# Kernel optimization log

Hardware: AMD Instinct MI355X
Metric: run time of the kernel (lower is better)

The kernel has to match this reference:

```python
import jax, jax.numpy as jnp
import numpy as np

NUM_GROUPS = 32
EPS = 1e-5


def setup_inputs() -> dict:
    key = jax.random.key(0)
    ks = jax.random.split(key, 6)
    B, C, H, W = 8, 128, 64, 64
    d = C // 8
    x = jax.random.normal(ks[0], (B, C, H, W), dtype=jnp.float32)
    # conv 1x1 weights stored as [out_ch, in_ch]; scaled like torch kaiming-uniform-ish
    s = 1.0 / np.sqrt(C)
    return {
        "x": x,
        "gn_w": jnp.ones((C,), jnp.float32),
        "gn_b": jnp.zeros((C,), jnp.float32),
        "q_w": jax.random.normal(ks[1], (d, C), jnp.float32) * s,
        "q_b": jnp.zeros((d,), jnp.float32),
        "k_w": jax.random.normal(ks[2], (d, C), jnp.float32) * s,
        "k_b": jnp.zeros((d,), jnp.float32),
        "v_w": jax.random.normal(ks[3], (C, C), jnp.float32) * s,
        "v_b": jnp.zeros((C,), jnp.float32),
        "p_w": jax.random.normal(ks[4], (C, C), jnp.float32) * s,
        "p_b": jnp.zeros((C,), jnp.float32),
    }


def _group_norm(x, w, b):
    B, C, H, W = x.shape
    g = NUM_GROUPS
    xr = x.reshape(B, g, C // g, H, W)
    mu = xr.mean(axis=(2, 3, 4), keepdims=True)
    var = xr.var(axis=(2, 3, 4), keepdims=True)
    xn = ((xr - mu) * jax.lax.rsqrt(var + EPS)).reshape(B, C, H, W)
    return xn * w[None, :, None, None] + b[None, :, None, None]


def reference(x, gn_w, gn_b, q_w, q_b, k_w, k_b, v_w, v_b, p_w, p_b):
    B, C, H, W = x.shape
    N = H * W
    h_ = _group_norm(x, gn_w, gn_b)            # [B,C,H,W]
    hf = h_.reshape(B, C, N)                   # flatten spatial
    # 1x1 convs == channel matmuls
    q = jnp.einsum('dc,bcn->bnd', q_w, hf) + q_b[None, None, :]   # [B,N,d]
    k = jnp.einsum('dc,bcn->bnd', k_w, hf) + k_b[None, None, :]   # [B,N,d]
    v = jnp.einsum('ec,bcn->ben', v_w, hf) + v_b[None, :, None]   # [B,C,N]
    d = q.shape[-1]
    scale = jnp.asarray(int(d) ** (-0.5), x.dtype)
    attn = jnp.einsum('bid,bjd->bij', q, k) * scale               # [B,N,N]
    attn = jax.nn.softmax(attn, axis=-1)
    a = jnp.einsum('bcj,bij->bci', v, attn)                       # [B,C,N]
    proj = jnp.einsum('ec,bcn->ben', p_w, a) + p_b[None, :, None]
    return x + proj.reshape(B, C, H, W)
```

## Files before the change

kernel.cpp:

```cpp
#include <hip/hip_runtime.h>
#include <math.h>


typedef short v8s __attribute__((ext_vector_type(8)));
typedef float v16f __attribute__((ext_vector_type(16)));

__device__ __forceinline__ unsigned short f2bf_rne(float f) {
  unsigned u = __float_as_uint(f);
  u += 0x7fffu + ((u >> 16) & 1u);
  return (unsigned short)(u >> 16);
}

__device__ __forceinline__ v8s mk8(unsigned a, unsigned b, unsigned c, unsigned d) {
  union { unsigned u[4]; v8s s; } x;
  x.u[0] = a; x.u[1] = b; x.u[2] = c; x.u[3] = d;
  return x.s;
}

__device__ __forceinline__ unsigned pack_trunc(float hi, float lo) {
  return __builtin_amdgcn_perm(__float_as_uint(hi), __float_as_uint(lo), 0x07060302u);
}

__device__ __forceinline__ void cp16_async(const unsigned short* g, unsigned short* l) {
  __builtin_amdgcn_global_load_lds(
      (const __attribute__((address_space(1))) unsigned int*)g,
      (__attribute__((address_space(3))) unsigned int*)l, 16, 0, 0);
}

#define VT(b, n, c) (((((size_t)(b) * 256 + ((n) >> 4)) << 7) + (c)) * 16 + ((n) & 15))

#define WSB_MURS   0u
#define WSB_WCATB  4096u
#define WSB_BCAT   49152u
#define WSB_PWB    65536u
#define WSB_QBF    131072u
#define WSB_KBF    1310720u
#define WSB_VBF    2621440u
#define WSB_ABF    11534336u

__global__ __launch_bounds__(512)
void gnprep_kernel(const float* __restrict__ x, float* __restrict__ mu_rs,
                   const float* __restrict__ qw, const float* __restrict__ qb,
                   const float* __restrict__ kw, const float* __restrict__ kb,
                   const float* __restrict__ vw, const float* __restrict__ vb,
                   const float* __restrict__ pw,
                   unsigned short* __restrict__ wcatb, float* __restrict__ bcat,
                   unsigned short* __restrict__ pwb) {
  const int id = blockIdx.x;
  {
    const float qs = 0.36067376022224085f;
    int idx = id * 512 + threadIdx.x;
    if (idx < 160 * 128) {
      int o = idx >> 7, c = idx & 127;
      float val;
      if (o < 16)       val = qw[o * 128 + c] * qs;
      else if (o < 32)  val = kw[(o - 16) * 128 + c];
      else              val = vw[(o - 32) * 128 + c];
      wcatb[idx] = f2bf_rne(val);
    } else if (idx < 160 * 128 + 160) {
      int o = idx - 160 * 128;
      bcat[o] = (o < 16) ? qb[o] * qs : (o < 32) ? kb[o - 16] : vb[o - 32];
    } else if (idx < 160 * 128 + 160 + 128 * 128) {
      int j = idx - (160 * 128 + 160);
      pwb[j] = f2bf_rne(pw[j]);
    }
  }
  const int bg = (id & 7) * 32 + (id >> 3);
  const float4* xp = (const float4*)(x + (size_t)bg * 16384);
  float s = 0.f, ss = 0.f;
#pragma unroll
  for (int u = 0; u < 8; ++u) {
    int i = threadIdx.x + u * 512;
    float4 v = xp[i];
    s  += v.x + v.y + v.z + v.w;
    ss += v.x * v.x + v.y * v.y + v.z * v.z + v.w * v.w;
  }
  for (int off = 32; off > 0; off >>= 1) {
    s  += __shfl_down(s, off, 64);
    ss += __shfl_down(ss, off, 64);
  }
  __shared__ float red[16];
  int lane = threadIdx.x & 63, wid = threadIdx.x >> 6;
  if (lane == 0) { red[wid * 2] = s; red[wid * 2 + 1] = ss; }
  __syncthreads();
  if (threadIdx.x == 0) {
    float S = 0.f, SS = 0.f;
    for (int w = 0; w < 8; ++w) { S += red[w * 2]; SS += red[w * 2 + 1]; }
    float mu  = S * (1.0f / 16384.0f);
    float var = SS * (1.0f / 16384.0f) - mu * mu;
    float rs  = rsqrtf(var + 1e-5f);
    mu_rs[bg * 2]     = mu;
    mu_rs[bg * 2 + 1] = rs;
  }
}

__global__ __launch_bounds__(512)
void qkv_kernel(const float* __restrict__ x, const float* __restrict__ gnw,
                const float* __restrict__ gnb, const float* __restrict__ mu_rs,
                const unsigned short* __restrict__ wcatb, const float* __restrict__ bcat,
                unsigned short* __restrict__ qTb, unsigned short* __restrict__ kbf,
                unsigned short* __restrict__ vbf) {
  __shared__ float scs[128], shs[128], bsh[160];
  const int id = blockIdx.x;
  const int b = id & 7, nb = (id >> 3) << 6;
  const int t = threadIdx.x;
  const int w = t >> 6, lane = t & 63, h = lane >> 5, l = lane & 31;
  const int nsub = w & 1, og = w >> 1;
  if (t < 128) {
    float mu = mu_rs[(b * 32 + (t >> 2)) * 2];
    float rs = mu_rs[(b * 32 + (t >> 2)) * 2 + 1];
    float gw = gnw[t], gb = gnb[t];
    scs[t] = rs * gw; shs[t] = gb - mu * rs * gw;
  }
  if (t < 160) bsh[t] = bcat[t];
  __syncthreads();

  const int n = nb + nsub * 32 + l;
  const float* xb = x + ((size_t)b * 128 << 12);
  const int otbase = (og == 0) ? 0 : og + 1;

  float xv[64];
#pragma unroll
  for (int ks = 0; ks < 8; ++ks)
#pragma unroll
    for (int p = 0; p < 8; ++p)
      xv[ks * 8 + p] = xb[((size_t)(ks * 16 + 8 * h + p) << 12) + n];

  v16f acc[2];
#pragma unroll
  for (int a2 = 0; a2 < 2; ++a2)
#pragma unroll
    for (int r = 0; r < 16; ++r) acc[a2][r] = 0.f;

#pragma unroll
  for (int ks = 0; ks < 8; ++ks) {
    const int c0 = ks * 16 + 8 * h;
    unsigned fd[4];
#pragma unroll
    for (int p = 0; p < 4; ++p) {
      int ca = c0 + 2 * p;
      float h0 = xv[ks * 8 + 2 * p]     * scs[ca]     + shs[ca];
      float h1 = xv[ks * 8 + 2 * p + 1] * scs[ca + 1] + shs[ca + 1];
      fd[p] = (unsigned)f2bf_rne(h0) | ((unsigned)f2bf_rne(h1) << 16);
    }
    v8s bf = mk8(fd[0], fd[1], fd[2], fd[3]);
    {
      v8s af = *(const v8s*)(wcatb + (otbase * 32 + l) * 128 + ks * 16 + 8 * h);
      acc[0] = __builtin_amdgcn_mfma_f32_32x32x16_bf16(af, bf, acc[0], 0, 0, 0);
    }
    if (og == 0) {
      v8s af = *(const v8s*)(wcatb + (32 + l) * 128 + ks * 16 + 8 * h);
      acc[1] = __builtin_amdgcn_mfma_f32_32x32x16_bf16(af, bf, acc[1], 0, 0, 0);
    }
  }

  if (og == 0) {
    const size_t nqk = ((size_t)b * 4096 + n) << 4;
#pragma unroll
    for (int r = 0; r < 16; ++r) {
      int o = 4 * h + (r & 3) + 8 * (r >> 2);
      unsigned short bv = f2bf_rne(acc[0][r] + bsh[o]);
      if (o < 16) qTb[((size_t)(b * 16 + o) << 12) + n] = bv;
      else        kbf[nqk + o - 16] = bv;
    }
#pragma unroll
    for (int r = 0; r < 16; ++r) {
      int o = 32 + 4 * h + (r & 3) + 8 * (r >> 2);
      vbf[VT(b, n, o - 32)] = f2bf_rne(acc[1][r] + bsh[o]);
    }
  } else {
#pragma unroll
    for (int r = 0; r < 16; ++r) {
      int o = otbase * 32 + 4 * h + (r & 3) + 8 * (r >> 2);
      vbf[VT(b, n, o - 32)] = f2bf_rne(acc[0][r] + bsh[o]);
    }
  }
}

__global__ __launch_bounds__(256)
void attn_kernel(const unsigned short* __restrict__ qTb,
                 const unsigned short* __restrict__ kbf,
                 const unsigned short* __restrict__ vbf,
                 unsigned short* __restrict__ abf) {
  __shared__ alignas(16) unsigned short smem[2][8192];
  __shared__ float l_lds[64];

  const int id = blockIdx.x;
  const int b = id & 7, i0 = (id >> 3) << 6;
  const int t = threadIdx.x;
  const int w = t >> 6, lane = t & 63, h = lane >> 5, l = lane & 31;
  const int jsub = w & 1, ihalf = w >> 1;

  const unsigned short* kg = kbf + ((size_t)b << 16);
  const unsigned short* vg = vbf + ((size_t)b << 19);

  const int iglob = i0 + ihalf * 32 + l;
  unsigned qd[4];
#pragma unroll
  for (int e = 0; e < 4; ++e) {
    unsigned lo = qTb[((size_t)(b * 16 + 8 * h + 2 * e) << 12) + iglob];
    unsigned hi = qTb[((size_t)(b * 16 + 8 * h + 2 * e + 1) << 12) + iglob];
    qd[e] = lo | (hi << 16);
  }
  const v8s qf = mk8(qd[0], qd[1], qd[2], qd[3]);

  v16f zc;
#pragma unroll
  for (int r = 0; r < 16; ++r) zc[r] = 0.f;
  v16f acc[4];
#pragma unroll
  for (int ct = 0; ct < 4; ++ct)
#pragma unroll
    for (int r = 0; r < 16; ++r) acc[ct][r] = 0.f;
  float ls = 0.f;

  if (t < 64) l_lds[t] = 0.f;

#pragma unroll
  for (int u = 0; u < 4; ++u)
    cp16_async(vg + (size_t)(w * 2048 + u * 512) + lane * 8,
               &smem[0][w * 2048 + u * 512]);
  __syncthreads();

  for (int tile = 0; tile < 64; ++tile) {
    const int tn = (tile + 1) & 63;
    unsigned short* const cur = smem[tile & 1];
    unsigned short* const nxt = smem[(tile + 1) & 1];

#pragma unroll
    for (int u = 0; u < 4; ++u)
      cp16_async(vg + (size_t)tn * 8192 + (w * 2048 + u * 512) + lane * 8,
                 &nxt[w * 2048 + u * 512]);

    v8s kf = *(const v8s*)(kg + (((size_t)(tile * 64 + jsub * 32 + l)) << 4) + 8 * h);

    v16f st = __builtin_amdgcn_mfma_f32_32x32x16_bf16(kf, qf, zc, 0, 0, 0);
    float pe[16];
#pragma unroll
    for (int r = 0; r < 16; ++r) { pe[r] = __builtin_amdgcn_exp2f(st[r]); ls += pe[r]; }
    unsigned G[8];
#pragma unroll
    for (int g = 0; g < 4; ++g) {
      G[2 * g]     = pack_trunc(pe[4 * g + 1], pe[4 * g]);
      G[2 * g + 1] = pack_trunc(pe[4 * g + 3], pe[4 * g + 2]);
    }
    unsigned S0 = h ? G[0] : G[2], S1 = h ? G[1] : G[3];
    unsigned S2 = h ? G[4] : G[6], S3 = h ? G[5] : G[7];
    unsigned R0 = (unsigned)__shfl_xor((int)S0, 32, 64);
    unsigned R1 = (unsigned)__shfl_xor((int)S1, 32, 64);
    unsigned R2 = (unsigned)__shfl_xor((int)S2, 32, 64);
    unsigned R3 = (unsigned)__shfl_xor((int)S3, 32, 64);
    v8s pf0 = h ? mk8(R0, R1, G[2], G[3]) : mk8(G[0], G[1], R0, R1);
    v8s pf1 = h ? mk8(R2, R3, G[6], G[7]) : mk8(G[4], G[5], R2, R3);

#pragma unroll
    for (int ct = 0; ct < 4; ++ct) {
      v8s vf0 = *(const v8s*)(&cur[((jsub * 2) * 128 + ct * 32 + l) * 16 + 8 * h]);
      v8s vf1 = *(const v8s*)(&cur[((jsub * 2 + 1) * 128 + ct * 32 + l) * 16 + 8 * h]);
      acc[ct] = __builtin_amdgcn_mfma_f32_32x32x16_bf16(vf0, pf0, acc[ct], 0, 0, 0);
      acc[ct] = __builtin_amdgcn_mfma_f32_32x32x16_bf16(vf1, pf1, acc[ct], 0, 0, 0);
    }

    __syncthreads();
  }

  atomicAdd(&l_lds[ihalf * 32 + l], ls);
  __syncthreads();
  float* const ov = (float*)smem;
  const float li = 1.f / l_lds[ihalf * 32 + l];
#pragma unroll
  for (int pass = 0; pass < 2; ++pass) {
    const int cta = pass * 2, ctb = pass * 2 + 1;
    if (jsub == 1) {
#pragma unroll
      for (int k = 0; k < 2; ++k) {
        const int ct = pass * 2 + k;
#pragma unroll
        for (int q = 0; q < 4; ++q) {
          float4 v4 = {acc[ct][4 * q], acc[ct][4 * q + 1],
                       acc[ct][4 * q + 2], acc[ct][4 * q + 3]};
          *(float4*)&ov[((k * 2 + ihalf) * 32 + l) * 36 + 4 * h + 8 * q] = v4;
        }
      }
    }
    __syncthreads();
    if (jsub == 0) {
#pragma unroll
      for (int k = 0; k < 2; ++k) {
        const int ct = pass * 2 + k;
#pragma unroll
        for (int q = 0; q < 4; ++q) {
          float4 v4 = *(float4*)&ov[((k * 2 + ihalf) * 32 + l) * 36 + 4 * h + 8 * q];
          acc[ct][4 * q]     += v4.x;
          acc[ct][4 * q + 1] += v4.y;
          acc[ct][4 * q + 2] += v4.z;
          acc[ct][4 * q + 3] += v4.w;
        }
#pragma unroll
        for (int r = 0; r < 16; ++r) {
          int c = ct * 32 + 4 * h + (r & 3) + 8 * (r >> 2);
          abf[((size_t)(b * 128 + c) << 12) + (size_t)(i0 + ihalf * 32 + l)] =
              f2bf_rne(acc[ct][r] * li);
        }
      }
    }
    __syncthreads();
  }
}

__global__ __launch_bounds__(512)
void proj_kernel(const unsigned short* __restrict__ abf, const unsigned short* __restrict__ pwb,
                 const float* __restrict__ pb, const float* __restrict__ x,
                 float* __restrict__ out) {
  __shared__ float pbs[128];
  const int id = blockIdx.x;
  const int b = id & 7, nb = (id >> 3) << 6;
  const int t = threadIdx.x;
  const int w = t >> 6, lane = t & 63, h = lane >> 5, l = lane & 31;
  const int nsub = w & 1, ot = w >> 1;
  if (t < 128) pbs[t] = pb[t];
  __syncthreads();

  const int n = nb + nsub * 32 + l;
  const unsigned short* ab = abf + (((size_t)b * 128) << 12);

  unsigned short av[64];
#pragma unroll
  for (int ks = 0; ks < 8; ++ks)
#pragma unroll
    for (int p = 0; p < 8; ++p)
      av[ks * 8 + p] = ab[((size_t)(ks * 16 + 8 * h + p) << 12) + n];

  v16f acc;
#pragma unroll
  for (int r = 0; r < 16; ++r) acc[r] = 0.f;

#pragma unroll
  for (int ks = 0; ks < 8; ++ks) {
    unsigned fd[4];
#pragma unroll
    for (int p = 0; p < 4; ++p)
      fd[p] = (unsigned)av[ks * 8 + 2 * p] | ((unsigned)av[ks * 8 + 2 * p + 1] << 16);
    v8s bf = mk8(fd[0], fd[1], fd[2], fd[3]);
    v8s af = *(const v8s*)(pwb + (ot * 32 + l) * 128 + ks * 16 + 8 * h);
    acc = __builtin_amdgcn_mfma_f32_32x32x16_bf16(af, bf, acc, 0, 0, 0);
  }

#pragma unroll
  for (int r = 0; r < 16; ++r) {
    int e = ot * 32 + 4 * h + (r & 3) + 8 * (r >> 2);
    size_t idx = ((size_t)(b * 128 + e) << 12) + n;
    out[idx] = acc[r] + pbs[e] + x[idx];
  }
}

extern "C" void kernel_launch(void* const* d_in, const int* in_sizes, int n_in,
                              void* d_out, int out_size, void* d_ws, size_t ws_size,
                              hipStream_t stream) {
  const float* x   = (const float*)d_in[0];
  const float* gnw = (const float*)d_in[1];
  const float* gnb = (const float*)d_in[2];
  const float* qw  = (const float*)d_in[3];
  const float* qb  = (const float*)d_in[4];
  const float* kw  = (const float*)d_in[5];
  const float* kb  = (const float*)d_in[6];
  const float* vw  = (const float*)d_in[7];
  const float* vb  = (const float*)d_in[8];
  const float* pw  = (const float*)d_in[9];
  const float* pb  = (const float*)d_in[10];
  float* out = (float*)d_out;
  char* ws = (char*)d_ws;

  float* mu_rs = (float*)(ws + WSB_MURS);
  unsigned short* wcatb = (unsigned short*)(ws + WSB_WCATB);
  float* bcat = (float*)(ws + WSB_BCAT);
  unsigned short* pwb = (unsigned short*)(ws + WSB_PWB);
  unsigned short* qTb = (unsigned short*)(ws + WSB_QBF);
  unsigned short* kbf = (unsigned short*)(ws + WSB_KBF);
  unsigned short* vbf = (unsigned short*)(ws + WSB_VBF);
  unsigned short* abf = (unsigned short*)(ws + WSB_ABF);

  hipLaunchKernelGGL(gnprep_kernel, dim3(256), dim3(512), 0, stream,
                     x, mu_rs, qw, qb, kw, kb, vw, vb, pw, wcatb, bcat, pwb);
  hipLaunchKernelGGL(qkv_kernel, dim3(512), dim3(512), 0, stream,
                     x, gnw, gnb, mu_rs, wcatb, bcat, qTb, kbf, vbf);
  hipLaunchKernelGGL(attn_kernel, dim3(512), dim3(256), 0, stream,
                     qTb, kbf, vbf, abf);
  hipLaunchKernelGGL(proj_kernel, dim3(512), dim3(512), 0, stream,
                     abf, pwb, pb, x, out);
}
```

Before: 172.6 us.

## Restructure attention to share V tiles across query halves and reblock A layout

The attention kernel now has each wave process both 32-row query halves against its own 32-key slice, with 128-key tiles staged through padded LDS using register loads instead of async global-to-LDS copies. The goal is to reuse each V fragment across two MFMAs, halve the tile count and avoid bank conflicts. The final reduction across the four waves now uses LDS float atomics. The intermediate attention output is stored in a channel-blocked layout (8 channels contiguous per position), so the projection kernel can load v8s fragments directly instead of making scattered 2-byte loads. In exchange, the kernel keeps twice as many accumulators live (register pressure), loses the double-buffered prefetch overlap, and pays for the atomic reduction.

```diff
diff --git a/kernel.cpp b/kernel.cpp
--- a/kernel.cpp
+++ b/kernel.cpp
@@ -21,13 +21,8 @@
   return __builtin_amdgcn_perm(__float_as_uint(hi), __float_as_uint(lo), 0x07060302u);
 }
 
-__device__ __forceinline__ void cp16_async(const unsigned short* g, unsigned short* l) {
-  __builtin_amdgcn_global_load_lds(
-      (const __attribute__((address_space(1))) unsigned int*)g,
-      (__attribute__((address_space(3))) unsigned int*)l, 16, 0, 0);
-}
-
 #define VT(b, n, c) (((((size_t)(b) * 256 + ((n) >> 4)) << 7) + (c)) * 16 + ((n) & 15))
+#define AB(b, c, n) ((((size_t)((b) * 16 + ((c) >> 3)) << 12) + (n)) * 8 + ((c) & 7))
 
 #define WSB_MURS   0u
 #define WSB_WCATB  4096u
@@ -177,134 +172,151 @@
   }
 }
 
+#define VSD 20
+
 __global__ __launch_bounds__(256)
 void attn_kernel(const unsigned short* __restrict__ qTb,
                  const unsigned short* __restrict__ kbf,
                  const unsigned short* __restrict__ vbf,
                  unsigned short* __restrict__ abf) {
-  __shared__ alignas(16) unsigned short smem[2][8192];
+  __shared__ alignas(16) unsigned short vlds[1024 * VSD];
   __shared__ float l_lds[64];
+  float* const ov = (float*)vlds;
 
   const int id = blockIdx.x;
   const int b = id & 7, i0 = (id >> 3) << 6;
   const int t = threadIdx.x;
   const int w = t >> 6, lane = t & 63, h = lane >> 5, l = lane & 31;
-  const int jsub = w & 1, ihalf = w >> 1;
 
   const unsigned short* kg = kbf + ((size_t)b << 16);
   const unsigned short* vg = vbf + ((size_t)b << 19);
 
-  const int iglob = i0 + ihalf * 32 + l;
-  unsigned qd[4];
+  unsigned qd0[4], qd1[4];
 #pragma unroll
   for (int e = 0; e < 4; ++e) {
-    unsigned lo = qTb[((size_t)(b * 16 + 8 * h + 2 * e) << 12) + iglob];
-    unsigned hi = qTb[((size_t)(b * 16 + 8 * h + 2 * e + 1) << 12) + iglob];
-    qd[e] = lo | (hi << 16);
-  }
-  const v8s qf = mk8(qd[0], qd[1], qd[2], qd[3]);
+    size_t rowa = (size_t)(b * 16 + 8 * h + 2 * e) << 12;
+    size_t rowb = (size_t)(b * 16 + 8 * h + 2 * e + 1) << 12;
+    unsigned lo0 = qTb[rowa + i0 + l],      hi0 = qTb[rowb + i0 + l];
+    unsigned lo1 = qTb[rowa + i0 + 32 + l], hi1 = qTb[rowb + i0 + 32 + l];
+    qd0[e] = lo0 | (hi0 << 16);
+    qd1[e] = lo1 | (hi1 << 16);
+  }
+  const v8s qf0 = mk8(qd0[0], qd0[1], qd0[2], qd0[3]);
+  const v8s qf1 = mk8(qd1[0], qd1[1], qd1[2], qd1[3]);
 
   v16f zc;
 #pragma unroll
   for (int r = 0; r < 16; ++r) zc[r] = 0.f;
-  v16f acc[4];
+  v16f acc[4][2];
 #pragma unroll
   for (int ct = 0; ct < 4; ++ct)
 #pragma unroll
-    for (int r = 0; r < 16; ++r) acc[ct][r] = 0.f;
-  float ls = 0.f;
+    for (int ih = 0; ih < 2; ++ih)
+#pragma unroll
+      for (int r = 0; r < 16; ++r) acc[ct][ih][r] = 0.f;
+  float ls0 = 0.f, ls1 = 0.f;
+
+  const int sc = t >> 1, shalf = (t & 1) * 8;
 
   if (t < 64) l_lds[t] = 0.f;
 
-#pragma unroll
-  for (int u = 0; u < 4; ++u)
-    cp16_async(vg + (size_t)(w * 2048 + u * 512) + lane * 8,
-               &smem[0][w * 2048 + u * 512]);
-  __syncthreads();
-
-  for (int tile = 0; tile < 64; ++tile) {
-    const int tn = (tile + 1) & 63;
-    unsigned short* const cur = smem[tile & 1];
-    unsigned short* const nxt = smem[(tile + 1) & 1];
-
-#pragma unroll
-    for (int u = 0; u < 4; ++u)
-      cp16_async(vg + (size_t)tn * 8192 + (w * 2048 + u * 512) + lane * 8,
-                 &nxt[w * 2048 + u * 512]);
-
-    v8s kf = *(const v8s*)(kg + (((size_t)(tile * 64 + jsub * 32 + l)) << 4) + 8 * h);
-
-    v16f st = __builtin_amdgcn_mfma_f32_32x32x16_bf16(kf, qf, zc, 0, 0, 0);
-    float pe[16];
-#pragma unroll
-    for (int r = 0; r < 16; ++r) { pe[r] = __builtin_amdgcn_exp2f(st[r]); ls += pe[r]; }
-    unsigned G[8];
-#pragma unroll
-    for (int g = 0; g < 4; ++g) {
-      G[2 * g]     = pack_trunc(pe[4 * g + 1], pe[4 * g]);
-      G[2 * g + 1] = pack_trunc(pe[4 * g + 3], pe[4 * g + 2]);
-    }
-    unsigned S0 = h ? G[0] : G[2], S1 = h ? G[1] : G[3];
-    unsigned S2 = h ? G[4] : G[6], S3 = h ? G[5] : G[7];
-    unsigned R0 = (unsigned)__shfl_xor((int)S0, 32, 64);
-    unsigned R1 = (unsigned)__shfl_xor((int)S1, 32, 64);
-    unsigned R2 = (unsigned)__shfl_xor((int)S2, 32, 64);
-    unsigned R3 = (unsigned)__shfl_xor((int)S3, 32, 64);
-    v8s pf0 = h ? mk8(R0, R1, G[2], G[3]) : mk8(G[0], G[1], R0, R1);
-    v8s pf1 = h ? mk8(R2, R3, G[6], G[7]) : mk8(G[4], G[5], R2, R3);
-
-#pragma unroll
-    for (int ct = 0; ct < 4; ++ct) {
-      v8s vf0 = *(const v8s*)(&cur[((jsub * 2) * 128 + ct * 32 + l) * 16 + 8 * h]);
-      v8s vf1 = *(const v8s*)(&cur[((jsub * 2 + 1) * 128 + ct * 32 + l) * 16 + 8 * h]);
-      acc[ct] = __builtin_amdgcn_mfma_f32_32x32x16_bf16(vf0, pf0, acc[ct], 0, 0, 0);
-      acc[ct] = __builtin_amdgcn_mfma_f32_32x32x16_bf16(vf1, pf1, acc[ct], 0, 0, 0);
-    }
+  for (int tile = 0; tile < 32; ++tile) {
+    v8s s[8];
+#pragma unroll
+    for (int u = 0; u < 8; ++u)
+      s[u] = *(const v8s*)(vg + (size_t)tile * 16384 + u * 2048 + sc * 16 + shalf);
+    v8s kf = *(const v8s*)(kg + (((size_t)(tile * 128 + w * 32 + l)) << 4) + 8 * h);
 
     __syncthreads();
-  }
-
-  atomicAdd(&l_lds[ihalf * 32 + l], ls);
-  __syncthreads();
-  float* const ov = (float*)smem;
-  const float li = 1.f / l_lds[ihalf * 32 + l];
-#pragma unroll
-  for (int pass = 0; pass < 2; ++pass) {
-    const int cta = pass * 2, ctb = pass * 2 + 1;
-    if (jsub == 1) {
-#pragma unroll
-      for (int k = 0; k < 2; ++k) {
-        const int ct = pass * 2 + k;
-#pragma unroll
-        for (int q = 0; q < 4; ++q) {
-          float4 v4 = {acc[ct][4 * q], acc[ct][4 * q + 1],
-                       acc[ct][4 * q + 2], acc[ct][4 * q + 3]};
-          *(float4*)&ov[((k * 2 + ihalf) * 32 + l) * 36 + 4 * h + 8 * q] = v4;
-        }
+
+#pragma unroll
+    for (int u = 0; u < 8; ++u)
+      *(v8s*)(&vlds[(u * 128 + sc) * VSD + shalf]) = s[u];
+
+    v16f st0 = __builtin_amdgcn_mfma_f32_32x32x16_bf16(kf, qf0, zc, 0, 0, 0);
+    v16f st1 = __builtin_amdgcn_mfma_f32_32x32x16_bf16(kf, qf1, zc, 0, 0, 0);
+    v8s pf[2][2];
+    {
+      float pe[16];
+#pragma unroll
+      for (int r = 0; r < 16; ++r) { pe[r] = __builtin_amdgcn_exp2f(st0[r]); ls0 += pe[r]; }
+      unsigned G[8];
+#pragma unroll
+      for (int g = 0; g < 4; ++g) {
+        G[2 * g]     = pack_trunc(pe[4 * g + 1], pe[4 * g]);
+        G[2 * g + 1] = pack_trunc(pe[4 * g + 3], pe[4 * g + 2]);
       }
-    }
+      unsigned S0 = h ? G[0] : G[2], S1 = h ? G[1] : G[3];
+      unsigned S2 = h ? G[4] : G[6], S3 = h ? G[5] : G[7];
+      unsigned R0 = (unsigned)__shfl_xor((int)S0, 32, 64);
+      unsigned R1 = (unsigned)__shfl_xor((int)S1, 32, 64);
+      unsigned R2 = (unsigned)__shfl_xor((int)S2, 32, 64);
+      unsigned R3 = (unsigned)__shfl_xor((int)S3, 32, 64);
+      pf[0][0] = h ? mk8(R0, R1, G[2], G[3]) : mk8(G[0], G[1], R0, R1);
+      pf[0][1] = h ? mk8(R2, R3, G[6], G[7]) : mk8(G[4], G[5], R2, R3);
+    }
+    {
+      float pe[16];
+#pragma unroll
+      for (int r = 0; r < 16; ++r) { pe[r] = __builtin_amdgcn_exp2f(st1[r]); ls1 += pe[r]; }
+      unsigned G[8];
+#pragma unroll
+      for (int g = 0; g < 4; ++g) {
+        G[2 * g]     = pack_trunc(pe[4 * g + 1], pe[4 * g]);
+        G[2 * g + 1] = pack_trunc(pe[4 * g + 3], pe[4 * g + 2]);
+      }
+      unsigned S0 = h ? G[0] : G[2], S1 = h ? G[1] : G[3];
+      unsigned S2 = h ? G[4] : G[6], S3 = h ? G[5] : G[7];
+      unsigned R0 = (unsigned)__shfl_xor((int)S0, 32, 64);
+      unsigned R1 = (unsigned)__shfl_xor((int)S1, 32, 64);
+      unsigned R2 = (unsigned)__shfl_xor((int)S2, 32, 64);
+      unsigned R3 = (unsigned)__shfl_xor((int)S3, 32, 64);
+      pf[1][0] = h ? mk8(R0, R1, G[2], G[3]) : mk8(G[0], G[1], R0, R1);
+      pf[1][1] = h ? mk8(R2, R3, G[6], G[7]) : mk8(G[4], G[5], R2, R3);
+    }
+
     __syncthreads();
-    if (jsub == 0) {
-#pragma unroll
-      for (int k = 0; k < 2; ++k) {
-        const int ct = pass * 2 + k;
-#pragma unroll
-        for (int q = 0; q < 4; ++q) {
-          float4 v4 = *(float4*)&ov[((k * 2 + ihalf) * 32 + l) * 36 + 4 * h + 8 * q];
-          acc[ct][4 * q]     += v4.x;
-          acc[ct][4 * q + 1] += v4.y;
-          acc[ct][4 * q + 2] += v4.z;
-          acc[ct][4 * q + 3] += v4.w;
-        }
-#pragma unroll
-        for (int r = 0; r < 16; ++r) {
-          int c = ct * 32 + 4 * h + (r & 3) + 8 * (r >> 2);
-          abf[((size_t)(b * 128 + c) << 12) + (size_t)(i0 + ihalf * 32 + l)] =
-              f2bf_rne(acc[ct][r] * li);
-        }
+
+#pragma unroll
+    for (int ks = 0; ks < 2; ++ks)
+#pragma unroll
+      for (int ct = 0; ct < 4; ++ct) {
+        v8s vf = *(const v8s*)(&vlds[((w * 2 + ks) * 128 + ct * 32 + l) * VSD + 8 * h]);
+        acc[ct][0] = __builtin_amdgcn_mfma_f32_32x32x16_bf16(vf, pf[0][ks], acc[ct][0], 0, 0, 0);
+        acc[ct][1] = __builtin_amdgcn_mfma_f32_32x32x16_bf16(vf, pf[1][ks], acc[ct][1], 0, 0, 0);
       }
-    }
-    __syncthreads();
+  }
+
+  atomicAdd(&l_lds[l], ls0);
+  atomicAdd(&l_lds[32 + l], ls1);
+  __syncthreads();
+
+  for (int idx = t; idx < 9216; idx += 256) ov[idx] = 0.f;
+  __syncthreads();
+#pragma unroll
+  for (int ct = 0; ct < 4; ++ct)
+#pragma unroll
+    for (int ih = 0; ih < 2; ++ih)
+#pragma unroll
+      for (int r = 0; r < 16; ++r)
+        atomicAdd(&ov[((ct * 2 + ih) * 32 + l) * 36 + 4 * h + (r & 3) + 8 * (r >> 2)],
+                  acc[ct][ih][r]);
+  __syncthreads();
+
+  {
+    const int g = t >> 5, i = t & 31;
+    const int ct = g >> 1, ih = g & 1;
+    const int n = i0 + ih * 32 + i;
+    const float li = 1.f / l_lds[ih * 32 + i];
+#pragma unroll
+    for (int m = 0; m < 8; ++m) {
+      float4 v4 = *(float4*)&ov[(g * 32 + i) * 36 + 4 * m];
+      int c = ct * 32 + 4 * m;
+      unsigned d0 = (unsigned)f2bf_rne(v4.x * li) | ((unsigned)f2bf_rne(v4.y * li) << 16);
+      unsigned d1 = (unsigned)f2bf_rne(v4.z * li) | ((unsigned)f2bf_rne(v4.w * li) << 16);
+      uint2 st2; st2.x = d0; st2.y = d1;
+      *(uint2*)(abf + AB(b, c, n)) = st2;
+    }
   }
 }
 
@@ -322,14 +334,11 @@
   __syncthreads();
 
   const int n = nb + nsub * 32 + l;
-  const unsigned short* ab = abf + (((size_t)b * 128) << 12);
-
-  unsigned short av[64];
+
+  v8s bfr[8];
 #pragma unroll
   for (int ks = 0; ks < 8; ++ks)
-#pragma unroll
-    for (int p = 0; p < 8; ++p)
-      av[ks * 8 + p] = ab[((size_t)(ks * 16 + 8 * h + p) << 12) + n];
+    bfr[ks] = *(const v8s*)(abf + ((((size_t)(b * 16 + ks * 2 + h)) << 12) + n) * 8);
 
   v16f acc;
 #pragma unroll
@@ -337,13 +346,8 @@
 
 #pragma unroll
   for (int ks = 0; ks < 8; ++ks) {
-    unsigned fd[4];
-#pragma unroll
-    for (int p = 0; p < 4; ++p)
-      fd[p] = (unsigned)av[ks * 8 + 2 * p] | ((unsigned)av[ks * 8 + 2 * p + 1] << 16);
-    v8s bf = mk8(fd[0], fd[1], fd[2], fd[3]);
     v8s af = *(const v8s*)(pwb + (ot * 32 + l) * 128 + ks * 16 + 8 * h);
-    acc = __builtin_amdgcn_mfma_f32_32x32x16_bf16(af, bf, acc, 0, 0, 0);
+    acc = __builtin_amdgcn_mfma_f32_32x32x16_bf16(af, bfr[ks], acc, 0, 0, 0);
   }
 
 #pragma unroll
```

After: 269.1 us. 1.56x slower.
